# Performance work log

Hardware: AMD Instinct MI355X
Metric: run time of the kernel (lower is better)

## Reference

```python
import jax, jax.numpy as jnp
import numpy as np

K, Q, DIM = 64, 128, 1024
TF_W, DE_W, FFT_W = 1.0, 0.8, 0.6  # opt.TF_weight / DE_weight / FFT_weight


def setup_inputs() -> dict:
    key = jax.random.key(0)
    ks = jax.random.split(key, 9)
    def feats(k):
        return jax.random.normal(k, (K, Q, DIM), dtype=jnp.float32)
    def protos(k):
        return jax.random.normal(k, (K, DIM), dtype=jnp.float32)
    def var(k):
        # positive variances, bounded away from zero
        return jax.random.uniform(k, (K,), dtype=jnp.float32) + 0.5
    return {
        "TFq_output": feats(ks[0]), "TFs_proto": protos(ks[1]), "TF_variance": var(ks[2]),
        "DEq_output": feats(ks[3]), "DEs_proto": protos(ks[4]), "DE_variance": var(ks[5]),
        "FFTq_output": feats(ks[6]), "FFTs_proto": protos(ks[7]), "FFT_variance": var(ks[8]),
    }


def _mah_dist(xq, proto, variance):
    # ||x - p||^2 / var via expansion: avoids materializing (num, protonum, dim)
    x2 = jnp.sum(xq * xq, axis=1, keepdims=True)            # (num, 1)
    p2 = jnp.sum(proto * proto, axis=1)[None, :]            # (1, protonum)
    xp = xq @ proto.T                                       # (num, protonum)
    return (x2 - 2.0 * xp + p2) / variance[None, :]


def _modality(xq, proto, variance, w):
    logits = -_mah_dist(xq, proto, variance)
    pred = w * jax.nn.softmax(logits, axis=1)
    mahloss = -(w * jax.nn.log_softmax(logits, axis=1))
    return pred, mahloss


def reference(TFq_output, TFs_proto, TF_variance,
              DEq_output, DEs_proto, DE_variance,
              FFTq_output, FFTs_proto, FFT_variance):
    k, q, _ = TFq_output.shape
    y = jnp.repeat(jnp.arange(k), q)                         # (k*q,)

    tf_pred, tf_loss = _modality(TFq_output.reshape(k * q, -1), TFs_proto, TF_variance, TF_W)
    de_pred, de_loss = _modality(DEq_output.reshape(k * q, -1), DEs_proto, DE_variance, DE_W)
    fft_pred, fft_loss = _modality(FFTq_output.reshape(k * q, -1), FFTs_proto, FFT_variance, FFT_W)

    fusion_loss = tf_loss + de_loss + fft_loss               # (k*q, k)
    loss = jnp.take_along_axis(fusion_loss, y[:, None], axis=1).squeeze(-1).mean()

    pred_mah = tf_pred + de_pred + fft_pred
    pred = jnp.argmax(pred_mah, axis=1)
    acc = (pred == y).astype(jnp.float32).mean()
    return (loss, acc)
```

## Files before the change

kernel.cpp:

```cpp
#include <hip/hip_runtime.h>


typedef _Float16 half8 __attribute__((ext_vector_type(8)));
typedef float    floatx4 __attribute__((ext_vector_type(4)));

#define NCLS   64
#define QPC    128
#define DIM    1024
#define NROWS  (NCLS * QPC)
#define KSPLIT 4
#define KSLICE (DIM / KSPLIT)
#define NITER  (KSLICE / 32)
#define NWAVES 12
#define NBLK   (NROWS / 16)
#define DSTRIDE 17
#define PSTRIDE 65

#define WPROTO_BYTES (3 * NCLS * DIM * 2)
#define P2_BYTES     (3 * NCLS * 4)
#define PART_BYTES   (NBLK * 2 * 4)
#define WS_NEED      (WPROTO_BYTES + P2_BYTES + PART_BYTES)

__global__ __launch_bounds__(64) void prep_protos(
    const float* __restrict__ Ptf, const float* __restrict__ Pde,
    const float* __restrict__ Pff, _Float16* __restrict__ W,
    float* __restrict__ p2)
{
    const int m    = blockIdx.x >> 5;
    const int kcg  = blockIdx.x & 31;
    const int lane = threadIdx.x;
    const int l15  = lane & 15;
    const int quad = lane >> 4;
    const float* __restrict__ P = (m == 0) ? Ptf : (m == 1) ? Pde : Pff;

    #pragma unroll
    for (int t = 0; t < 4; ++t) {
        const float* src = P + (size_t)(t * 16 + l15) * DIM + kcg * 32 + quad * 8;
        const float4 b0 = *reinterpret_cast<const float4*>(src);
        const float4 b1 = *reinterpret_cast<const float4*>(src + 4);
        half8 h;
        h[0] = (_Float16)b0.x; h[1] = (_Float16)b0.y;
        h[2] = (_Float16)b0.z; h[3] = (_Float16)b0.w;
        h[4] = (_Float16)b1.x; h[5] = (_Float16)b1.y;
        h[6] = (_Float16)b1.z; h[7] = (_Float16)b1.w;
        *reinterpret_cast<half8*>(W + ((size_t)(m * 32 + kcg) * 4 + t) * 512 + lane * 8) = h;

        float s = b0.x*b0.x + b0.y*b0.y + b0.z*b0.z + b0.w*b0.w
                + b1.x*b1.x + b1.y*b1.y + b1.z*b1.z + b1.w*b1.w;
        s += __shfl_xor(s, 16);
        s += __shfl_xor(s, 32);
        if (quad == 0) atomicAdd(&p2[m * 64 + t * 16 + l15], s);
    }
}

__global__ __launch_bounds__(NWAVES * 64, 3) void fusion_loss_kernel(
    const float* __restrict__ Xtf, const float* __restrict__ Vtf,
    const float* __restrict__ Xde, const float* __restrict__ Vde,
    const float* __restrict__ Xff, const float* __restrict__ Vff,
    const _Float16* __restrict__ W, const float* __restrict__ p2g,
    float2* __restrict__ partial)
{
    __shared__ float dpart[NWAVES][64 * DSTRIDE];
    __shared__ float x2part[NWAVES][16];
    __shared__ float predL[16 * PSTRIDE];
    __shared__ float lossL;

    const int tid  = threadIdx.x;
    const int wave = tid >> 6;
    const int lane = tid & 63;
    const int l15  = lane & 15;
    const int quad = lane >> 4;
    const int m    = wave >> 2;
    const int kq   = wave & 3;
    const int rowBase = blockIdx.x * 16;

    for (int i = tid; i < 16 * PSTRIDE; i += NWAVES * 64) predL[i] = 0.0f;
    if (tid == 0) lossL = 0.0f;

    const float* __restrict__ X = (m == 0) ? Xtf : (m == 1) ? Xde : Xff;
    const float* __restrict__ V = (m == 0) ? Vtf : (m == 1) ? Vde : Vff;
    const float  w = (m == 0) ? 1.0f : (m == 1) ? 0.8f : 0.6f;

    const float* xrow = X + (size_t)(rowBase + l15) * DIM + kq * KSLICE + quad * 8;
    float4 abuf[2 * NITER];
    #pragma unroll
    for (int kc = 0; kc < NITER; ++kc) {
        abuf[2 * kc]     = *reinterpret_cast<const float4*>(xrow + kc * 32);
        abuf[2 * kc + 1] = *reinterpret_cast<const float4*>(xrow + kc * 32 + 4);
    }

    const _Float16* wbase = W + (size_t)(m * 32 + kq * NITER) * 4 * 512 + lane * 8;

    floatx4 d[4];
    #pragma unroll
    for (int t = 0; t < 4; ++t) d[t] = (floatx4){0.f, 0.f, 0.f, 0.f};
    float x2p = 0.0f;

    #pragma unroll
    for (int kc = 0; kc < NITER; ++kc) {
        half8 bf[4];
        #pragma unroll
        for (int t = 0; t < 4; ++t)
            bf[t] = *reinterpret_cast<const half8*>(wbase + (size_t)(kc * 4 + t) * 512);

        const float4 a0 = abuf[2 * kc];
        const float4 a1 = abuf[2 * kc + 1];
        x2p += a0.x*a0.x + a0.y*a0.y + a0.z*a0.z + a0.w*a0.w
             + a1.x*a1.x + a1.y*a1.y + a1.z*a1.z + a1.w*a1.w;

        half8 af;
        af[0] = (_Float16)a0.x; af[1] = (_Float16)a0.y;
        af[2] = (_Float16)a0.z; af[3] = (_Float16)a0.w;
        af[4] = (_Float16)a1.x; af[5] = (_Float16)a1.y;
        af[6] = (_Float16)a1.z; af[7] = (_Float16)a1.w;

        #pragma unroll
        for (int t = 0; t < 4; ++t)
            d[t] = __builtin_amdgcn_mfma_f32_16x16x32_f16(af, bf[t], d[t], 0, 0, 0);
    }

    x2p += __shfl_xor(x2p, 16);
    x2p += __shfl_xor(x2p, 32);

    {
        float* dp = &dpart[wave][lane * DSTRIDE];
        #pragma unroll
        for (int t = 0; t < 4; ++t)
            *reinterpret_cast<float4*>(dp + t * 4) =
                make_float4(d[t][0], d[t][1], d[t][2], d[t][3]);
        if (quad == 0) x2part[wave][l15] = x2p;
    }
    __syncthreads();

    const int y = rowBase >> 7;

    if (kq == 0) {
        floatx4 dsum[4];
        #pragma unroll
        for (int t = 0; t < 4; ++t) dsum[t] = (floatx4){0.f, 0.f, 0.f, 0.f};
        float x2r[4] = {0.f, 0.f, 0.f, 0.f};
        #pragma unroll
        for (int k2 = 0; k2 < KSPLIT; ++k2) {
            const int wv = m * 4 + k2;
            const float* src = &dpart[wv][lane * DSTRIDE];
            #pragma unroll
            for (int t = 0; t < 4; ++t) {
                const float4 v = *reinterpret_cast<const float4*>(src + t * 4);
                dsum[t][0] += v.x; dsum[t][1] += v.y; dsum[t][2] += v.z; dsum[t][3] += v.w;
            }
            #pragma unroll
            for (int r = 0; r < 4; ++r) x2r[r] += x2part[wv][quad * 4 + r];
        }
        float vc[4], p2c[4];
        #pragma unroll
        for (int t = 0; t < 4; ++t) {
            vc[t]  = V[t * 16 + l15];
            p2c[t] = p2g[m * 64 + t * 16 + l15];
        }

        float lossAcc = 0.0f;
        #pragma unroll
        for (int r = 0; r < 4; ++r) {
            float lg[4];
            #pragma unroll
            for (int t = 0; t < 4; ++t)
                lg[t] = (2.0f * dsum[t][r] - x2r[r] - p2c[t]) / vc[t];

            float mx = fmaxf(fmaxf(lg[0], lg[1]), fmaxf(lg[2], lg[3]));
            #pragma unroll
            for (int dl = 1; dl <= 8; dl <<= 1) mx = fmaxf(mx, __shfl_xor(mx, dl));
            float s = expf(lg[0] - mx) + expf(lg[1] - mx)
                    + expf(lg[2] - mx) + expf(lg[3] - mx);
            #pragma unroll
            for (int dl = 1; dl <= 8; dl <<= 1) s += __shfl_xor(s, dl);
            const float lse = mx + logf(s);

            const int row = quad * 4 + r;
            #pragma unroll
            for (int t = 0; t < 4; ++t) {
                const int col = t * 16 + l15;
                if (col == y) lossAcc += w * (lse - lg[t]);
                atomicAdd(&predL[row * PSTRIDE + col], w * expf(lg[t] - lse));
            }
        }
        #pragma unroll
        for (int dl = 1; dl <= 32; dl <<= 1) lossAcc += __shfl_xor(lossAcc, dl);
        if (lane == 0) atomicAdd(&lossL, lossAcc);
    }
    __syncthreads();

    if (wave == 0) {
        float cnt = 0.0f;
        #pragma unroll 1
        for (int r = 0; r < 16; ++r) {
            float bv = predL[r * PSTRIDE + lane];
            int   bc = lane;
            #pragma unroll
            for (int dl = 1; dl <= 32; dl <<= 1) {
                const float ov = __shfl_xor(bv, dl);
                const int   oc = __shfl_xor(bc, dl);
                if (ov > bv || (ov == bv && oc < bc)) { bv = ov; bc = oc; }
            }
            if (lane == 0 && bc == y) cnt += 1.0f;
        }
        if (lane == 0) partial[blockIdx.x] = make_float2(lossL, cnt);
    }
}

__global__ __launch_bounds__(256) void finalize(
    const float2* __restrict__ partial, float* __restrict__ out)
{
    const int tid  = threadIdx.x;
    const int lane = tid & 63;
    const int wv   = tid >> 6;
    float l = 0.0f, c = 0.0f;
    for (int i = tid; i < NBLK; i += 256) {
        const float2 p = partial[i];
        l += p.x; c += p.y;
    }
    #pragma unroll
    for (int dl = 1; dl <= 32; dl <<= 1) {
        l += __shfl_xor(l, dl);
        c += __shfl_xor(c, dl);
    }
    __shared__ float sl[4], sc[4];
    if (lane == 0) { sl[wv] = l; sc[wv] = c; }
    __syncthreads();
    if (tid == 0) {
        out[0] = (sl[0] + sl[1] + sl[2] + sl[3]) * (1.0f / NROWS);
        out[1] = (sc[0] + sc[1] + sc[2] + sc[3]) * (1.0f / NROWS);
    }
}

__global__ __launch_bounds__(NWAVES * 64) void fusion_loss_fallback(
    const float* __restrict__ Xtf, const float* __restrict__ Ptf, const float* __restrict__ Vtf,
    const float* __restrict__ Xde, const float* __restrict__ Pde, const float* __restrict__ Vde,
    const float* __restrict__ Xff, const float* __restrict__ Pff, const float* __restrict__ Vff,
    float* __restrict__ out)
{
    __shared__ float dpart[NWAVES][64 * DSTRIDE];
    __shared__ float x2part[NWAVES][16];
    __shared__ float p2part[NWAVES][64];
    __shared__ float predL[16 * PSTRIDE];
    __shared__ float lossL;

    const int tid  = threadIdx.x;
    const int wave = tid >> 6;
    const int lane = tid & 63;
    const int l15  = lane & 15;
    const int quad = lane >> 4;
    const int m    = wave >> 2;
    const int kq   = wave & 3;
    const int rowBase = blockIdx.x * 16;

    for (int i = tid; i < 16 * PSTRIDE; i += NWAVES * 64) predL[i] = 0.0f;
    if (tid == 0) lossL = 0.0f;

    const float* __restrict__ X = (m == 0) ? Xtf : (m == 1) ? Xde : Xff;
    const float* __restrict__ P = (m == 0) ? Ptf : (m == 1) ? Pde : Pff;
    const float* __restrict__ V = (m == 0) ? Vtf : (m == 1) ? Vde : Vff;
    const float  w = (m == 0) ? 1.0f : (m == 1) ? 0.8f : 0.6f;

    floatx4 d[4];
    #pragma unroll
    for (int t = 0; t < 4; ++t) d[t] = (floatx4){0.f, 0.f, 0.f, 0.f};
    float x2p    = 0.0f;
    float p2p[4] = {0.f, 0.f, 0.f, 0.f};

    const float* xrow = X + (size_t)(rowBase + l15) * DIM + kq * KSLICE + quad * 8;
    const float* prow[4];
    #pragma unroll
    for (int t = 0; t < 4; ++t)
        prow[t] = P + (size_t)(t * 16 + l15) * DIM + kq * KSLICE + quad * 8;

    #pragma unroll 2
    for (int kc = 0; kc < NITER; ++kc) {
        const int ko = kc * 32;
        const float4 a0 = *reinterpret_cast<const float4*>(xrow + ko);
        const float4 a1 = *reinterpret_cast<const float4*>(xrow + ko + 4);
        float4 b0[4], b1[4];
        #pragma unroll
        for (int t = 0; t < 4; ++t) {
            b0[t] = *reinterpret_cast<const float4*>(prow[t] + ko);
            b1[t] = *reinterpret_cast<const float4*>(prow[t] + ko + 4);
        }
        x2p += a0.x*a0.x + a0.y*a0.y + a0.z*a0.z + a0.w*a0.w
             + a1.x*a1.x + a1.y*a1.y + a1.z*a1.z + a1.w*a1.w;
        half8 af;
        af[0] = (_Float16)a0.x; af[1] = (_Float16)a0.y;
        af[2] = (_Float16)a0.z; af[3] = (_Float16)a0.w;
        af[4] = (_Float16)a1.x; af[5] = (_Float16)a1.y;
        af[6] = (_Float16)a1.z; af[7] = (_Float16)a1.w;
        #pragma unroll
        for (int t = 0; t < 4; ++t) {
            p2p[t] += b0[t].x*b0[t].x + b0[t].y*b0[t].y + b0[t].z*b0[t].z + b0[t].w*b0[t].w
                    + b1[t].x*b1[t].x + b1[t].y*b1[t].y + b1[t].z*b1[t].z + b1[t].w*b1[t].w;
            half8 bf;
            bf[0] = (_Float16)b0[t].x; bf[1] = (_Float16)b0[t].y;
            bf[2] = (_Float16)b0[t].z; bf[3] = (_Float16)b0[t].w;
            bf[4] = (_Float16)b1[t].x; bf[5] = (_Float16)b1[t].y;
            bf[6] = (_Float16)b1[t].z; bf[7] = (_Float16)b1[t].w;
            d[t] = __builtin_amdgcn_mfma_f32_16x16x32_f16(af, bf, d[t], 0, 0, 0);
        }
    }

    x2p += __shfl_xor(x2p, 16);
    x2p += __shfl_xor(x2p, 32);
    #pragma unroll
    for (int t = 0; t < 4; ++t) {
        p2p[t] += __shfl_xor(p2p[t], 16);
        p2p[t] += __shfl_xor(p2p[t], 32);
    }
    {
        float* dp = &dpart[wave][lane * DSTRIDE];
        #pragma unroll
        for (int t = 0; t < 4; ++t)
            *reinterpret_cast<float4*>(dp + t * 4) =
                make_float4(d[t][0], d[t][1], d[t][2], d[t][3]);
        if (quad == 0) {
            x2part[wave][l15] = x2p;
            #pragma unroll
            for (int t = 0; t < 4; ++t) p2part[wave][t * 16 + l15] = p2p[t];
        }
    }
    __syncthreads();

    const int y = rowBase >> 7;

    if (kq == 0) {
        floatx4 dsum[4];
        #pragma unroll
        for (int t = 0; t < 4; ++t) dsum[t] = (floatx4){0.f, 0.f, 0.f, 0.f};
        float x2r[4] = {0.f, 0.f, 0.f, 0.f};
        float p2c[4] = {0.f, 0.f, 0.f, 0.f};
        #pragma unroll
        for (int k2 = 0; k2 < KSPLIT; ++k2) {
            const int wv = m * 4 + k2;
            const float* src = &dpart[wv][lane * DSTRIDE];
            #pragma unroll
            for (int t = 0; t < 4; ++t) {
                const float4 v = *reinterpret_cast<const float4*>(src + t * 4);
                dsum[t][0] += v.x; dsum[t][1] += v.y; dsum[t][2] += v.z; dsum[t][3] += v.w;
            }
            #pragma unroll
            for (int r = 0; r < 4; ++r) x2r[r] += x2part[wv][quad * 4 + r];
            #pragma unroll
            for (int t = 0; t < 4; ++t) p2c[t] += p2part[wv][t * 16 + l15];
        }
        float vc[4];
        #pragma unroll
        for (int t = 0; t < 4; ++t) vc[t] = V[t * 16 + l15];

        float lossAcc = 0.0f;
        #pragma unroll
        for (int r = 0; r < 4; ++r) {
            float lg[4];
            #pragma unroll
            for (int t = 0; t < 4; ++t)
                lg[t] = (2.0f * dsum[t][r] - x2r[r] - p2c[t]) / vc[t];
            float mx = fmaxf(fmaxf(lg[0], lg[1]), fmaxf(lg[2], lg[3]));
            #pragma unroll
            for (int dl = 1; dl <= 8; dl <<= 1) mx = fmaxf(mx, __shfl_xor(mx, dl));
            float s = expf(lg[0] - mx) + expf(lg[1] - mx)
                    + expf(lg[2] - mx) + expf(lg[3] - mx);
            #pragma unroll
            for (int dl = 1; dl <= 8; dl <<= 1) s += __shfl_xor(s, dl);
            const float lse = mx + logf(s);
            const int row = quad * 4 + r;
            #pragma unroll
            for (int t = 0; t < 4; ++t) {
                const int col = t * 16 + l15;
                if (col == y) lossAcc += w * (lse - lg[t]);
                atomicAdd(&predL[row * PSTRIDE + col], w * expf(lg[t] - lse));
            }
        }
        #pragma unroll
        for (int dl = 1; dl <= 32; dl <<= 1) lossAcc += __shfl_xor(lossAcc, dl);
        if (lane == 0) atomicAdd(&lossL, lossAcc);
    }
    __syncthreads();

    if (wave == 0) {
        float cnt = 0.0f;
        #pragma unroll 1
        for (int r = 0; r < 16; ++r) {
            float bv = predL[r * PSTRIDE + lane];
            int   bc = lane;
            #pragma unroll
            for (int dl = 1; dl <= 32; dl <<= 1) {
                const float ov = __shfl_xor(bv, dl);
                const int   oc = __shfl_xor(bc, dl);
                if (ov > bv || (ov == bv && oc < bc)) { bv = ov; bc = oc; }
            }
            if (lane == 0 && bc == y) cnt += 1.0f;
        }
        if (lane == 0) {
            atomicAdd(&out[0], lossL * (1.0f / NROWS));
            atomicAdd(&out[1], cnt * (1.0f / NROWS));
        }
    }
}

extern "C" void kernel_launch(void* const* d_in, const int* in_sizes, int n_in,
                              void* d_out, int out_size, void* d_ws, size_t ws_size,
                              hipStream_t stream) {
    const float* Xtf = (const float*)d_in[0];
    const float* Ptf = (const float*)d_in[1];
    const float* Vtf = (const float*)d_in[2];
    const float* Xde = (const float*)d_in[3];
    const float* Pde = (const float*)d_in[4];
    const float* Vde = (const float*)d_in[5];
    const float* Xff = (const float*)d_in[6];
    const float* Pff = (const float*)d_in[7];
    const float* Vff = (const float*)d_in[8];
    float* out = (float*)d_out;

    if (ws_size >= (size_t)WS_NEED) {
        _Float16* W    = (_Float16*)d_ws;
        float*    p2   = (float*)((char*)d_ws + WPROTO_BYTES);
        float2*   part = (float2*)((char*)d_ws + WPROTO_BYTES + P2_BYTES);
        hipMemsetAsync(p2, 0, P2_BYTES, stream);
        prep_protos<<<dim3(96), dim3(64), 0, stream>>>(Ptf, Pde, Pff, W, p2);
        fusion_loss_kernel<<<dim3(NBLK), dim3(NWAVES * 64), 0, stream>>>(
            Xtf, Vtf, Xde, Vde, Xff, Vff, W, p2, part);
        finalize<<<dim3(1), dim3(256), 0, stream>>>(part, out);
    } else {
        hipMemsetAsync(out, 0, 2 * sizeof(float), stream);
        fusion_loss_fallback<<<dim3(NBLK), dim3(NWAVES * 64), 0, stream>>>(
            Xtf, Ptf, Vtf, Xde, Pde, Vde, Xff, Pff, Vff, out);
    }
}
```

Before: 172.3 us.

## Split waves by output column tile and stage X rows via LDS DMA

```diff
diff --git a/kernel.cpp b/kernel.cpp
--- a/kernel.cpp
+++ b/kernel.cpp
@@ -8,18 +8,21 @@
 #define QPC    128
 #define DIM    1024
 #define NROWS  (NCLS * QPC)
-#define KSPLIT 4
-#define KSLICE (DIM / KSPLIT)
-#define NITER  (KSLICE / 32)
-#define NWAVES 12
-#define NBLK   (NROWS / 16)
-#define DSTRIDE 17
-#define PSTRIDE 65
-
-#define WPROTO_BYTES (3 * NCLS * DIM * 2)
-#define P2_BYTES     (3 * NCLS * 4)
-#define PART_BYTES   (NBLK * 2 * 4)
-#define WS_NEED      (WPROTO_BYTES + P2_BYTES + PART_BYTES)
+#define NRT    (NROWS / 16)
+#define UW     260
+
+#define OFF_W     0
+#define W_BYTES   (3 * NCLS * DIM * 2)
+#define OFF_P2    W_BYTES
+#define OFF_PART  394240
+#define WS_NEED   (OFF_PART + NRT * 8)
+
+__device__ __forceinline__ void dma16(const float* g, float* l) {
+    __builtin_amdgcn_global_load_lds(
+        (const __attribute__((address_space(1))) void*)g,
+        (__attribute__((address_space(3))) void*)l,
+        16, 0, 0);
+}
 
 __global__ __launch_bounds__(64) void prep_protos(
     const float* __restrict__ Ptf, const float* __restrict__ Pde,
@@ -53,16 +56,18 @@
     }
 }
 
-__global__ __launch_bounds__(NWAVES * 64, 3) void fusion_loss_kernel(
+__global__ __launch_bounds__(768, 6) void fusion_main(
     const float* __restrict__ Xtf, const float* __restrict__ Vtf,
     const float* __restrict__ Xde, const float* __restrict__ Vde,
     const float* __restrict__ Xff, const float* __restrict__ Vff,
     const _Float16* __restrict__ W, const float* __restrict__ p2g,
     float2* __restrict__ partial)
 {
-    __shared__ float dpart[NWAVES][64 * DSTRIDE];
-    __shared__ float x2part[NWAVES][16];
-    __shared__ float predL[16 * PSTRIDE];
+    __shared__ float tiles[3][16 * UW];
+    __shared__ float x2s[3][16];
+    __shared__ float mxW[12][16];
+    __shared__ float sW[12][16];
+    __shared__ float predL[16 * 65];
     __shared__ float lossL;
 
     const int tid  = threadIdx.x;
@@ -71,129 +76,107 @@
     const int l15  = lane & 15;
     const int quad = lane >> 4;
     const int m    = wave >> 2;
-    const int kq   = wave & 3;
+    const int t    = wave & 3;
     const int rowBase = blockIdx.x * 16;
 
-    for (int i = tid; i < 16 * PSTRIDE; i += NWAVES * 64) predL[i] = 0.0f;
+    for (int i = tid; i < 16 * 65; i += 768) predL[i] = 0.0f;
     if (tid == 0) lossL = 0.0f;
 
     const float* __restrict__ X = (m == 0) ? Xtf : (m == 1) ? Xde : Xff;
     const float* __restrict__ V = (m == 0) ? Vtf : (m == 1) ? Vde : Vff;
-    const float  w = (m == 0) ? 1.0f : (m == 1) ? 0.8f : 0.6f;
-
-    const float* xrow = X + (size_t)(rowBase + l15) * DIM + kq * KSLICE + quad * 8;
-    float4 abuf[2 * NITER];
-    #pragma unroll
-    for (int kc = 0; kc < NITER; ++kc) {
-        abuf[2 * kc]     = *reinterpret_cast<const float4*>(xrow + kc * 32);
-        abuf[2 * kc + 1] = *reinterpret_cast<const float4*>(xrow + kc * 32 + 4);
-    }
-
-    const _Float16* wbase = W + (size_t)(m * 32 + kq * NITER) * 4 * 512 + lane * 8;
-
-    floatx4 d[4];
-    #pragma unroll
-    for (int t = 0; t < 4; ++t) d[t] = (floatx4){0.f, 0.f, 0.f, 0.f};
+    const float  wgt = (m == 0) ? 1.0f : (m == 1) ? 0.8f : 0.6f;
+
+    floatx4 d = (floatx4){0.f, 0.f, 0.f, 0.f};
     float x2p = 0.0f;
 
-    #pragma unroll
-    for (int kc = 0; kc < NITER; ++kc) {
-        half8 bf[4];
-        #pragma unroll
-        for (int t = 0; t < 4; ++t)
-            bf[t] = *reinterpret_cast<const half8*>(wbase + (size_t)(kc * 4 + t) * 512);
-
-        const float4 a0 = abuf[2 * kc];
-        const float4 a1 = abuf[2 * kc + 1];
-        x2p += a0.x*a0.x + a0.y*a0.y + a0.z*a0.z + a0.w*a0.w
-             + a1.x*a1.x + a1.y*a1.y + a1.z*a1.z + a1.w*a1.w;
-
-        half8 af;
-        af[0] = (_Float16)a0.x; af[1] = (_Float16)a0.y;
-        af[2] = (_Float16)a0.z; af[3] = (_Float16)a0.w;
-        af[4] = (_Float16)a1.x; af[5] = (_Float16)a1.y;
-        af[6] = (_Float16)a1.z; af[7] = (_Float16)a1.w;
-
-        #pragma unroll
-        for (int t = 0; t < 4; ++t)
-            d[t] = __builtin_amdgcn_mfma_f32_16x16x32_f16(af, bf[t], d[t], 0, 0, 0);
-    }
-
-    x2p += __shfl_xor(x2p, 16);
-    x2p += __shfl_xor(x2p, 32);
-
-    {
-        float* dp = &dpart[wave][lane * DSTRIDE];
-        #pragma unroll
-        for (int t = 0; t < 4; ++t)
-            *reinterpret_cast<float4*>(dp + t * 4) =
-                make_float4(d[t][0], d[t][1], d[t][2], d[t][3]);
-        if (quad == 0) x2part[wave][l15] = x2p;
+    #pragma unroll 1
+    for (int c = 0; c < 4; ++c) {
+        if (c) __syncthreads();
+        const float* gb = X + (size_t)(rowBase + t * 4) * DIM + c * 256 + lane * 4;
+        #pragma unroll
+        for (int r4 = 0; r4 < 4; ++r4)
+            dma16(gb + (size_t)r4 * DIM, &tiles[m][(t * 4 + r4) * UW]);
+        __syncthreads();
+
+        #pragma unroll
+        for (int kc = 0; kc < 8; ++kc) {
+            const int off = l15 * UW + kc * 32 + quad * 8;
+            const float4 a0 = *reinterpret_cast<const float4*>(&tiles[m][off]);
+            const float4 a1 = *reinterpret_cast<const float4*>(&tiles[m][off + 4]);
+            const half8 bf = *reinterpret_cast<const half8*>(
+                W + ((size_t)(m * 32 + c * 8 + kc) * 4 + t) * 512 + lane * 8);
+
+            if (t == 0)
+                x2p += a0.x*a0.x + a0.y*a0.y + a0.z*a0.z + a0.w*a0.w
+                     + a1.x*a1.x + a1.y*a1.y + a1.z*a1.z + a1.w*a1.w;
+
+            half8 af;
+            af[0] = (_Float16)a0.x; af[1] = (_Float16)a0.y;
+            af[2] = (_Float16)a0.z; af[3] = (_Float16)a0.w;
+            af[4] = (_Float16)a1.x; af[5] = (_Float16)a1.y;
+            af[6] = (_Float16)a1.z; af[7] = (_Float16)a1.w;
+
+            d = __builtin_amdgcn_mfma_f32_16x16x32_f16(af, bf, d, 0, 0, 0);
+        }
+    }
+
+    if (t == 0) {
+        x2p += __shfl_xor(x2p, 16);
+        x2p += __shfl_xor(x2p, 32);
+        if (quad == 0) x2s[m][l15] = x2p;
+    }
+    __syncthreads();
+
+    const int col = t * 16 + l15;
+    const float vc  = V[col];
+    const float p2c = p2g[m * 64 + col];
+    float lg[4];
+    #pragma unroll
+    for (int r = 0; r < 4; ++r)
+        lg[r] = (2.0f * d[r] - x2s[m][quad * 4 + r] - p2c) / vc;
+
+    #pragma unroll
+    for (int r = 0; r < 4; ++r) {
+        float mx = lg[r];
+        #pragma unroll
+        for (int dl = 1; dl <= 8; dl <<= 1) mx = fmaxf(mx, __shfl_xor(mx, dl));
+        if (l15 == 0) mxW[wave][quad * 4 + r] = mx;
+    }
+    __syncthreads();
+
+    float gmx[4];
+    #pragma unroll
+    for (int r = 0; r < 4; ++r) {
+        const int row = quad * 4 + r;
+        gmx[r] = fmaxf(fmaxf(mxW[m * 4 + 0][row], mxW[m * 4 + 1][row]),
+                       fmaxf(mxW[m * 4 + 2][row], mxW[m * 4 + 3][row]));
+        float s = expf(lg[r] - gmx[r]);
+        #pragma unroll
+        for (int dl = 1; dl <= 8; dl <<= 1) s += __shfl_xor(s, dl);
+        if (l15 == 0) sW[wave][quad * 4 + r] = s;
     }
     __syncthreads();
 
     const int y = rowBase >> 7;
-
-    if (kq == 0) {
-        floatx4 dsum[4];
-        #pragma unroll
-        for (int t = 0; t < 4; ++t) dsum[t] = (floatx4){0.f, 0.f, 0.f, 0.f};
-        float x2r[4] = {0.f, 0.f, 0.f, 0.f};
-        #pragma unroll
-        for (int k2 = 0; k2 < KSPLIT; ++k2) {
-            const int wv = m * 4 + k2;
-            const float* src = &dpart[wv][lane * DSTRIDE];
-            #pragma unroll
-            for (int t = 0; t < 4; ++t) {
-                const float4 v = *reinterpret_cast<const float4*>(src + t * 4);
-                dsum[t][0] += v.x; dsum[t][1] += v.y; dsum[t][2] += v.z; dsum[t][3] += v.w;
-            }
-            #pragma unroll
-            for (int r = 0; r < 4; ++r) x2r[r] += x2part[wv][quad * 4 + r];
-        }
-        float vc[4], p2c[4];
-        #pragma unroll
-        for (int t = 0; t < 4; ++t) {
-            vc[t]  = V[t * 16 + l15];
-            p2c[t] = p2g[m * 64 + t * 16 + l15];
-        }
-
-        float lossAcc = 0.0f;
-        #pragma unroll
-        for (int r = 0; r < 4; ++r) {
-            float lg[4];
-            #pragma unroll
-            for (int t = 0; t < 4; ++t)
-                lg[t] = (2.0f * dsum[t][r] - x2r[r] - p2c[t]) / vc[t];
-
-            float mx = fmaxf(fmaxf(lg[0], lg[1]), fmaxf(lg[2], lg[3]));
-            #pragma unroll
-            for (int dl = 1; dl <= 8; dl <<= 1) mx = fmaxf(mx, __shfl_xor(mx, dl));
-            float s = expf(lg[0] - mx) + expf(lg[1] - mx)
-                    + expf(lg[2] - mx) + expf(lg[3] - mx);
-            #pragma unroll
-            for (int dl = 1; dl <= 8; dl <<= 1) s += __shfl_xor(s, dl);
-            const float lse = mx + logf(s);
-
-            const int row = quad * 4 + r;
-            #pragma unroll
-            for (int t = 0; t < 4; ++t) {
-                const int col = t * 16 + l15;
-                if (col == y) lossAcc += w * (lse - lg[t]);
-                atomicAdd(&predL[row * PSTRIDE + col], w * expf(lg[t] - lse));
-            }
-        }
-        #pragma unroll
-        for (int dl = 1; dl <= 32; dl <<= 1) lossAcc += __shfl_xor(lossAcc, dl);
-        if (lane == 0) atomicAdd(&lossL, lossAcc);
-    }
+    float lossAcc = 0.0f;
+    #pragma unroll
+    for (int r = 0; r < 4; ++r) {
+        const int row = quad * 4 + r;
+        const float lse = gmx[r] + logf(sW[m * 4 + 0][row] + sW[m * 4 + 1][row]
+                                      + sW[m * 4 + 2][row] + sW[m * 4 + 3][row]);
+        if (col == y) lossAcc += wgt * (lse - lg[r]);
+        atomicAdd(&predL[row * 65 + col], wgt * expf(lg[r] - lse));
+    }
+    #pragma unroll
+    for (int dl = 1; dl <= 32; dl <<= 1) lossAcc += __shfl_xor(lossAcc, dl);
+    if (lane == 0) atomicAdd(&lossL, lossAcc);
     __syncthreads();
 
     if (wave == 0) {
         float cnt = 0.0f;
         #pragma unroll 1
         for (int r = 0; r < 16; ++r) {
-            float bv = predL[r * PSTRIDE + lane];
+            float bv = predL[r * 65 + lane];
             int   bc = lane;
             #pragma unroll
             for (int dl = 1; dl <= 32; dl <<= 1) {
@@ -212,9 +195,9 @@
 {
     const int tid  = threadIdx.x;
     const int lane = tid & 63;
-    const int wv   = tid >> 6;
+    const int v    = tid >> 6;
     float l = 0.0f, c = 0.0f;
-    for (int i = tid; i < NBLK; i += 256) {
+    for (int i = tid; i < NRT; i += 256) {
         const float2 p = partial[i];
         l += p.x; c += p.y;
     }
@@ -224,13 +207,20 @@
         c += __shfl_xor(c, dl);
     }
     __shared__ float sl[4], sc[4];
-    if (lane == 0) { sl[wv] = l; sc[wv] = c; }
+    if (lane == 0) { sl[v] = l; sc[v] = c; }
     __syncthreads();
     if (tid == 0) {
         out[0] = (sl[0] + sl[1] + sl[2] + sl[3]) * (1.0f / NROWS);
         out[1] = (sc[0] + sc[1] + sc[2] + sc[3]) * (1.0f / NROWS);
     }
 }
+
+#define NWAVES 12
+#define KSPLIT 4
+#define KSLICE (DIM / KSPLIT)
+#define NITER  (KSLICE / 32)
+#define DSTRIDE 17
+#define PSTRIDE 65
 
 __global__ __launch_bounds__(NWAVES * 64) void fusion_loss_fallback(
     const float* __restrict__ Xtf, const float* __restrict__ Ptf, const float* __restrict__ Vtf,
@@ -339,8 +329,8 @@
             const float* src = &dpart[wv][lane * DSTRIDE];
             #pragma unroll
             for (int t = 0; t < 4; ++t) {
-                const float4 v = *reinterpret_cast<const float4*>(src + t * 4);
-                dsum[t][0] += v.x; dsum[t][1] += v.y; dsum[t][2] += v.z; dsum[t][3] += v.w;
+                const float4 vv = *reinterpret_cast<const float4*>(src + t * 4);
+                dsum[t][0] += vv.x; dsum[t][1] += vv.y; dsum[t][2] += vv.z; dsum[t][3] += vv.w;
             }
             #pragma unroll
             for (int r = 0; r < 4; ++r) x2r[r] += x2part[wv][quad * 4 + r];
@@ -369,9 +359,9 @@
             const int row = quad * 4 + r;
             #pragma unroll
             for (int t = 0; t < 4; ++t) {
-                const int col = t * 16 + l15;
-                if (col == y) lossAcc += w * (lse - lg[t]);
-                atomicAdd(&predL[row * PSTRIDE + col], w * expf(lg[t] - lse));
+                const int colc = t * 16 + l15;
+                if (colc == y) lossAcc += w * (lse - lg[t]);
+                atomicAdd(&predL[row * PSTRIDE + colc], w * expf(lg[t] - lse));
             }
         }
         #pragma unroll
@@ -416,17 +406,19 @@
     float* out = (float*)d_out;
 
     if (ws_size >= (size_t)WS_NEED) {
-        _Float16* W    = (_Float16*)d_ws;
-        float*    p2   = (float*)((char*)d_ws + WPROTO_BYTES);
-        float2*   part = (float2*)((char*)d_ws + WPROTO_BYTES + P2_BYTES);
-        hipMemsetAsync(p2, 0, P2_BYTES, stream);
+        char* ws = (char*)d_ws;
+        _Float16* W    = (_Float16*)(ws + OFF_W);
+        float*    p2   = (float*)(ws + OFF_P2);
+        float2*   part = (float2*)(ws + OFF_PART);
+
+        hipMemsetAsync(p2, 0, 3 * NCLS * sizeof(float), stream);
         prep_protos<<<dim3(96), dim3(64), 0, stream>>>(Ptf, Pde, Pff, W, p2);
-        fusion_loss_kernel<<<dim3(NBLK), dim3(NWAVES * 64), 0, stream>>>(
+        fusion_main<<<dim3(NRT), dim3(768), 0, stream>>>(
             Xtf, Vtf, Xde, Vde, Xff, Vff, W, p2, part);
         finalize<<<dim3(1), dim3(256), 0, stream>>>(part, out);
     } else {
         hipMemsetAsync(out, 0, 2 * sizeof(float), stream);
-        fusion_loss_fallback<<<dim3(NBLK), dim3(NWAVES * 64), 0, stream>>>(
+        fusion_loss_fallback<<<dim3(NROWS / 16), dim3(NWAVES * 64), 0, stream>>>(
             Xtf, Ptf, Vtf, Xde, Pde, Vde, Xff, Pff, Vff, out);
     }
 }
```

After: 159.7 us. 1.08x faster.
